# Optimization experiments

Measured on AMD Instinct MI355X. Metric: run time of the kernel, lower is better.

The kernel has to match this reference:

```python
import jax, jax.numpy as jnp
import numpy as np

N_HEAD = 16


def setup_inputs() -> dict:
    key = jax.random.key(0)
    ks = jax.random.split(key, 6)
    B, S, D = 2, 2048, 1024
    w = 0.02
    return {
        "x": jax.random.normal(ks[0], (B, S, D), dtype=jnp.float32),
        "attention_mask": jnp.ones((B, S), dtype=jnp.int32),
        "Wq": jax.random.normal(ks[1], (D, D), dtype=jnp.float32) * w,
        "bq": jnp.zeros((D,), dtype=jnp.float32),
        "Wk": jax.random.normal(ks[2], (D, D), dtype=jnp.float32) * w,
        "bk": jnp.zeros((D,), dtype=jnp.float32),
        "Wv": jax.random.normal(ks[3], (D, D), dtype=jnp.float32) * w,
        "bv": jnp.zeros((D,), dtype=jnp.float32),
        "Wp": jax.random.normal(ks[4], (D, D), dtype=jnp.float32) * w,
        "bp": jnp.zeros((D,), dtype=jnp.float32),
    }


def reference(x, attention_mask, Wq, bq, Wk, bk, Wv, bv, Wp, bp):
    # x: (B,S,D); PyTorch Linear: y = x @ W.T + b
    B, S, D = x.shape
    H = N_HEAD
    HD = D // H
    scale = 1.0 / jnp.sqrt(jnp.asarray(HD, dtype=x.dtype))

    def heads(W, b):
        return (x @ W.T + b).reshape(B, S, H, HD).transpose(0, 2, 1, 3)  # (B,H,S,HD)

    q = heads(Wq, bq)
    k = heads(Wk, bk)
    v = heads(Wv, bv)

    logits = jnp.einsum("bhsd,bhtd->bhst", q, k) * scale  # (B,H,S,S)

    causal = jnp.tril(jnp.ones((S, S), dtype=bool))  # (S,S)
    am = attention_mask.astype(bool)
    mask = causal[None, None, :, :] & (am[:, None, :, None] & am[:, None, None, :])

    float_min = jnp.finfo(x.dtype).min
    logits = jnp.where(mask, logits, float_min)
    w = jax.nn.softmax(logits, axis=-1)  # dropout is identity in eval / p=0

    attn = jnp.einsum("bhst,bhtd->bhsd", w, v)  # (B,H,S,HD)
    attn = attn.transpose(0, 2, 1, 3).reshape(B, S, D)
    return attn @ Wp.T + bp
```

## Files before the change

kernel.cpp:

```cpp
#include <hip/hip_runtime.h>


#define BB 2
#define SS 2048
#define DD 1024
#define HH 16
#define HDD 64
#define NEG_BIG (-1.0e30f)

typedef __attribute__((ext_vector_type(8))) short short8;
typedef __attribute__((ext_vector_type(4))) float floatx4;
typedef unsigned int u32;
#define AS_GLOBAL __attribute__((address_space(1)))
#define AS_LDS    __attribute__((address_space(3)))

__device__ __forceinline__ ushort f2bf(float f) {
    unsigned u = __float_as_uint(f);
    u += 0x7fffu + ((u >> 16) & 1u);
    return (ushort)(u >> 16);
}
__device__ __forceinline__ unsigned pk2(float a, float b) {
    return ((unsigned)f2bf(b) << 16) | (unsigned)f2bf(a);
}
__device__ __forceinline__ void storeT(float* p, float v) { *p = v; }
__device__ __forceinline__ void storeT(ushort* p, float v) { *p = f2bf(v); }

__device__ __forceinline__ void dma16(void* lds, const void* g) {
    __builtin_amdgcn_global_load_lds((const AS_GLOBAL u32*)g, (AS_LDS u32*)lds,
                                     16, 0, 0);
}

__global__ __launch_bounds__(256) void cvt_all(
    const float* __restrict__ x, const float* __restrict__ wq,
    const float* __restrict__ wk, const float* __restrict__ wv,
    ushort* __restrict__ dst)
{
    const size_t g = (size_t)blockIdx.x * 256 + threadIdx.x;
    const size_t flat = g * 8;
    const float* s;
    size_t off;
    if (flat < (size_t)4194304)      { s = x;  off = flat; }
    else if (flat < (size_t)5242880) { s = wq; off = flat - 4194304; }
    else if (flat < (size_t)6291456) { s = wk; off = flat - 5242880; }
    else                             { s = wv; off = flat - 6291456; }
    const float4 a = ((const float4*)(s + off))[0];
    const float4 b = ((const float4*)(s + off))[1];
    uint4 u;
    u.x = pk2(a.x, a.y); u.y = pk2(a.z, a.w);
    u.z = pk2(b.x, b.y); u.w = pk2(b.z, b.w);
    *(uint4*)(dst + flat) = u;
}

template <int QKV, typename TW, typename TO>
__global__ __launch_bounds__(256) void gemm_mfma(
    const ushort* __restrict__ A,
    const TW* __restrict__ W0, const TW* __restrict__ W1,
    const TW* __restrict__ W2,
    const float* __restrict__ B0, const float* __restrict__ B1,
    const float* __restrict__ B2,
    TO* __restrict__ O0, TO* __restrict__ O1, TO* __restrict__ O2)
{
    __shared__ ushort As[128 * 32];
    __shared__ ushort Bs[128 * 32];
    __shared__ float bias_s[128];

    const TW* W;
    const float* bias;
    TO* out;
    int z = 0;
    if (QKV) {
        z = blockIdx.z;
        W    = z == 0 ? W0 : (z == 1 ? W1 : W2);
        bias = z == 0 ? B0 : (z == 1 ? B1 : B2);
        out  = z == 0 ? O0 : (z == 1 ? O1 : O2);
    } else { W = W0; bias = B0; out = O0; }

    const int tid = threadIdx.x;
    const int bm = blockIdx.x * 128, bn = blockIdx.y * 128;
    const int wave = tid >> 6, lane = tid & 63, quad = lane >> 4, lm = lane & 15;
    const int wm = wave >> 1, wn = wave & 1;
    const int r0 = tid >> 2, c0 = (tid & 3) * 8;

    if (tid < 128) bias_s[tid] = bias[bn + tid];

    const floatx4 zz = {0.f, 0.f, 0.f, 0.f};
    floatx4 acc[4][4];
#pragma unroll
    for (int i = 0; i < 4; ++i)
#pragma unroll
        for (int j = 0; j < 4; ++j) acc[i][j] = zz;

    for (int k0 = 0; k0 < DD; k0 += 32) {
        __syncthreads();
        dma16(&As[r0 * 32 + c0], A + (size_t)(bm + r0) * DD + k0 + c0);
        dma16(&As[(64 + r0) * 32 + c0], A + (size_t)(bm + 64 + r0) * DD + k0 + c0);
        if constexpr (sizeof(TW) == 2) {
            dma16(&Bs[r0 * 32 + c0],
                  (const ushort*)W + (size_t)(bn + r0) * DD + k0 + c0);
            dma16(&Bs[(64 + r0) * 32 + c0],
                  (const ushort*)W + (size_t)(bn + 64 + r0) * DD + k0 + c0);
        } else {
#pragma unroll
            for (int hh = 0; hh < 2; ++hh) {
                const float* wr = (const float*)W
                    + (size_t)(bn + hh * 64 + r0) * DD + k0 + c0;
                const float4 a = ((const float4*)wr)[0];
                const float4 b = ((const float4*)wr)[1];
                uint4 u;
                u.x = pk2(a.x, a.y); u.y = pk2(a.z, a.w);
                u.z = pk2(b.x, b.y); u.w = pk2(b.z, b.w);
                *(uint4*)&Bs[(hh * 64 + r0) * 32 + c0] = u;
            }
        }
        __syncthreads();

        short8 af[4], bf[4];
#pragma unroll
        for (int i = 0; i < 4; ++i)
            af[i] = *(const short8*)&As[(wm * 64 + i * 16 + lm) * 32 + quad * 8];
#pragma unroll
        for (int j = 0; j < 4; ++j)
            bf[j] = *(const short8*)&Bs[(wn * 64 + j * 16 + lm) * 32 + quad * 8];
#pragma unroll
        for (int i = 0; i < 4; ++i)
#pragma unroll
            for (int j = 0; j < 4; ++j)
                acc[i][j] = __builtin_amdgcn_mfma_f32_16x16x32_bf16(
                    af[i], bf[j], acc[i][j], 0, 0, 0);
    }

#pragma unroll
    for (int i = 0; i < 4; ++i) {
#pragma unroll
        for (int j = 0; j < 4; ++j) {
            const int nl = wn * 64 + j * 16 + lm;
            const int n = bn + nl;
            const float bb = bias_s[nl];
#pragma unroll
            for (int r = 0; r < 4; ++r) {
                const int m = bm + wm * 64 + i * 16 + quad * 4 + r;
                const float v = acc[i][j][r] + bb;
                size_t oidx;
                if (QKV) {
                    const int b = m >> 11, s = m & 2047, h = n >> 6, hd = n & 63;
                    if (z == 2)
                        oidx = (((size_t)(b * HH + h) * HDD) + hd) * SS + s;
                    else
                        oidx = (((size_t)(b * HH + h) * SS) + s) * HDD + hd;
                } else {
                    oidx = (size_t)m * DD + n;
                }
                storeT(out + oidx, v);
            }
        }
    }
}

__global__ __launch_bounds__(256) void attn_mfma(
    const ushort* __restrict__ Q, const ushort* __restrict__ K,
    const ushort* __restrict__ Vt, const int* __restrict__ am,
    ushort* __restrict__ O)
{
    __shared__ ushort Ks[64 * 72];
    __shared__ ushort Vts[64 * 72];
    __shared__ ushort Ps[4][32 * 72];

    const int tid = threadIdx.x;
    const int wq = tid >> 6, lane = tid & 63, quad = lane >> 4, lm = lane & 15;
    const int qt = (int)(gridDim.x - 1 - blockIdx.x);
    const int bh = blockIdx.y, b = bh >> 4, h = bh & 15;
    const size_t base = (size_t)bh * SS * HDD;
    const size_t tbase = (size_t)bh * HDD * SS;
    const int* amrow = am + b * SS;
    const int q0 = qt * 128 + wq * 32;

    short8 qf[2][2];
#pragma unroll
    for (int sub = 0; sub < 2; ++sub) {
        const ushort* qp = Q + base + (size_t)(q0 + sub * 16 + lm) * HDD + quad * 8;
        qf[sub][0] = *(const short8*)qp;
        qf[sub][1] = *(const short8*)(qp + 32);
    }
    int amq[2][4];
#pragma unroll
    for (int sub = 0; sub < 2; ++sub)
#pragma unroll
        for (int r = 0; r < 4; ++r)
            amq[sub][r] = amrow[q0 + sub * 16 + quad * 4 + r];

    const floatx4 zz = {0.f, 0.f, 0.f, 0.f};
    floatx4 o_acc[2][4];
#pragma unroll
    for (int sub = 0; sub < 2; ++sub)
#pragma unroll
        for (int n2 = 0; n2 < 4; ++n2) o_acc[sub][n2] = zz;
    float l_r[2][4] = {};

    const int sr = tid >> 2, sc = (tid & 3) * 16;
    const int ktmax = 2 * qt + 1;

    for (int kt = 0; kt <= ktmax; ++kt) {
        __syncthreads();
        {
            const ushort* kp = K + base + (size_t)(kt * 64 + sr) * HDD + sc;
            const uint4 u0 = ((const uint4*)kp)[0], u1 = ((const uint4*)kp)[1];
            *(uint4*)&Ks[sr * 72 + sc] = u0;
            *(uint4*)&Ks[sr * 72 + sc + 8] = u1;
        }
        {
            const ushort* vp = Vt + tbase + (size_t)sr * SS + kt * 64 + sc;
            const uint4 u0 = ((const uint4*)vp)[0], u1 = ((const uint4*)vp)[1];
            *(uint4*)&Vts[sr * 72 + sc] = u0;
            *(uint4*)&Vts[sr * 72 + sc + 8] = u1;
        }
        __syncthreads();

        int amk4[4];
#pragma unroll
        for (int nt = 0; nt < 4; ++nt) amk4[nt] = amrow[kt * 64 + nt * 16 + lm];

#pragma unroll
        for (int nt = 0; nt < 4; ++nt) {
            const short8 kf0 = *(const short8*)&Ks[(nt * 16 + lm) * 72 + quad * 8];
            const short8 kf1 = *(const short8*)&Ks[(nt * 16 + lm) * 72 + 32 + quad * 8];
            const int tg = kt * 64 + nt * 16 + lm;
#pragma unroll
            for (int sub = 0; sub < 2; ++sub) {
                floatx4 s = zz;
                s = __builtin_amdgcn_mfma_f32_16x16x32_bf16(qf[sub][0], kf0, s, 0, 0, 0);
                s = __builtin_amdgcn_mfma_f32_16x16x32_bf16(qf[sub][1], kf1, s, 0, 0, 0);
#pragma unroll
                for (int r = 0; r < 4; ++r) {
                    const int qg = q0 + sub * 16 + quad * 4 + r;
                    float sv = s[r] * 0.125f;
                    const bool ok = amk4[nt] && amq[sub][r] && (tg <= qg);
                    sv = ok ? sv : NEG_BIG;
                    const float e = __expf(fminf(sv, 30.f));
                    l_r[sub][r] += e;
                    Ps[wq][(sub * 16 + quad * 4 + r) * 72 + nt * 16 + lm] = f2bf(e);
                }
            }
        }

        short8 af[2][2];
#pragma unroll
        for (int sub = 0; sub < 2; ++sub) {
            af[sub][0] = *(const short8*)&Ps[wq][(sub * 16 + lm) * 72 + quad * 8];
            af[sub][1] = *(const short8*)&Ps[wq][(sub * 16 + lm) * 72 + 32 + quad * 8];
        }
#pragma unroll
        for (int n2 = 0; n2 < 4; ++n2) {
            const short8 vf0 = *(const short8*)&Vts[(n2 * 16 + lm) * 72 + quad * 8];
            const short8 vf1 = *(const short8*)&Vts[(n2 * 16 + lm) * 72 + 32 + quad * 8];
#pragma unroll
            for (int sub = 0; sub < 2; ++sub) {
                o_acc[sub][n2] = __builtin_amdgcn_mfma_f32_16x16x32_bf16(
                    af[sub][0], vf0, o_acc[sub][n2], 0, 0, 0);
                o_acc[sub][n2] = __builtin_amdgcn_mfma_f32_16x16x32_bf16(
                    af[sub][1], vf1, o_acc[sub][n2], 0, 0, 0);
            }
        }
    }

#pragma unroll
    for (int sub = 0; sub < 2; ++sub) {
        float inv[4];
#pragma unroll
        for (int r = 0; r < 4; ++r) {
            float l = l_r[sub][r];
            l += __shfl_xor(l, 1);
            l += __shfl_xor(l, 2);
            l += __shfl_xor(l, 4);
            l += __shfl_xor(l, 8);
            inv[r] = l > 0.f ? 1.f / l : 0.f;
        }
#pragma unroll
        for (int n2 = 0; n2 < 4; ++n2)
#pragma unroll
            for (int r = 0; r < 4; ++r) {
                const int s = q0 + sub * 16 + quad * 4 + r;
                O[((size_t)(b * SS + s)) * DD + h * HDD + n2 * 16 + lm] =
                    f2bf(o_acc[sub][n2][r] * inv[r]);
            }
    }
}

extern "C" void kernel_launch(void* const* d_in, const int* in_sizes, int n_in,
                              void* d_out, int out_size, void* d_ws, size_t ws_size,
                              hipStream_t stream) {
    const float* x  = (const float*)d_in[0];
    const int*   am = (const int*)d_in[1];
    const float* Wq = (const float*)d_in[2];
    const float* bq = (const float*)d_in[3];
    const float* Wk = (const float*)d_in[4];
    const float* bk = (const float*)d_in[5];
    const float* Wv = (const float*)d_in[6];
    const float* bv = (const float*)d_in[7];
    const float* Wp = (const float*)d_in[8];
    const float* bp = (const float*)d_in[9];
    float* out = (float*)d_out;

    const size_t elems = (size_t)BB * HH * SS * HDD;
    ushort* q_ws = (ushort*)d_ws;
    ushort* k_ws = q_ws + elems;
    ushort* v_ws = k_ws + elems;
    ushort* a_ws = v_ws + elems;

    ushort* xb  = (ushort*)d_out;
    ushort* wqb = xb + 4194304;
    ushort* wkb = wqb + 1048576;
    ushort* wvb = wkb + 1048576;

    cvt_all<<<3584, 256, 0, stream>>>(x, Wq, Wk, Wv, xb);

    gemm_mfma<1, ushort, ushort><<<dim3(32, 8, 3), 256, 0, stream>>>(
        xb, wqb, wkb, wvb, bq, bk, bv, q_ws, k_ws, v_ws);

    attn_mfma<<<dim3(SS / 128, BB * HH), 256, 0, stream>>>(q_ws, k_ws, v_ws, am, a_ws);

    gemm_mfma<0, float, float><<<dim3(32, 8, 1), 256, 0, stream>>>(
        a_ws, Wp, Wp, Wp, bp, bp, bp, out, out, out);
}
```

Before: 251.9 us.

## Split attention over key tiles into two partitions and add a combine kernel

Attention now splits each query tile's key loop across two blocks (even and odd key tiles). Each block writes an unnormalized partial output and row sums, and a new combine kernel sums the two partials and normalizes. This doubles the grid to improve occupancy and load balance, at the cost of an extra pass over partial outputs. The MFMA operands are also swapped so each lane holds 4 contiguous columns, which enables vectorized ushort4/float4 stores in the GEMM epilogues and attention output. The V projection is split into its own GEMM launch with a vectorized transposed store, and the key mask is staged through LDS.

```diff
diff --git a/kernel.cpp b/kernel.cpp
--- a/kernel.cpp
+++ b/kernel.cpp
@@ -22,9 +22,16 @@
 __device__ __forceinline__ unsigned pk2(float a, float b) {
     return ((unsigned)f2bf(b) << 16) | (unsigned)f2bf(a);
 }
-__device__ __forceinline__ void storeT(float* p, float v) { *p = v; }
-__device__ __forceinline__ void storeT(ushort* p, float v) { *p = f2bf(v); }
-
+__device__ __forceinline__ void unpack8(const uint4 u, float* d) {
+    d[0] = __uint_as_float(u.x << 16);
+    d[1] = __uint_as_float(u.x & 0xffff0000u);
+    d[2] = __uint_as_float(u.y << 16);
+    d[3] = __uint_as_float(u.y & 0xffff0000u);
+    d[4] = __uint_as_float(u.z << 16);
+    d[5] = __uint_as_float(u.z & 0xffff0000u);
+    d[6] = __uint_as_float(u.w << 16);
+    d[7] = __uint_as_float(u.w & 0xffff0000u);
+}
 __device__ __forceinline__ void dma16(void* lds, const void* g) {
     __builtin_amdgcn_global_load_lds((const AS_GLOBAL u32*)g, (AS_LDS u32*)lds,
                                      16, 0, 0);
@@ -35,8 +42,7 @@
     const float* __restrict__ wk, const float* __restrict__ wv,
     ushort* __restrict__ dst)
 {
-    const size_t g = (size_t)blockIdx.x * 256 + threadIdx.x;
-    const size_t flat = g * 8;
+    const size_t flat = ((size_t)blockIdx.x * 256 + threadIdx.x) * 8;
     const float* s;
     size_t off;
     if (flat < (size_t)4194304)      { s = x;  off = flat; }
@@ -51,29 +57,21 @@
     *(uint4*)(dst + flat) = u;
 }
 
-template <int QKV, typename TW, typename TO>
+template <int MODE, typename TW, typename TO>
 __global__ __launch_bounds__(256) void gemm_mfma(
     const ushort* __restrict__ A,
     const TW* __restrict__ W0, const TW* __restrict__ W1,
-    const TW* __restrict__ W2,
     const float* __restrict__ B0, const float* __restrict__ B1,
-    const float* __restrict__ B2,
-    TO* __restrict__ O0, TO* __restrict__ O1, TO* __restrict__ O2)
+    TO* __restrict__ O0, TO* __restrict__ O1)
 {
     __shared__ ushort As[128 * 32];
     __shared__ ushort Bs[128 * 32];
     __shared__ float bias_s[128];
 
-    const TW* W;
-    const float* bias;
-    TO* out;
-    int z = 0;
-    if (QKV) {
-        z = blockIdx.z;
-        W    = z == 0 ? W0 : (z == 1 ? W1 : W2);
-        bias = z == 0 ? B0 : (z == 1 ? B1 : B2);
-        out  = z == 0 ? O0 : (z == 1 ? O1 : O2);
-    } else { W = W0; bias = B0; out = O0; }
+    const TW* W = W0;
+    const float* bias = B0;
+    TO* out = O0;
+    if (MODE == 1 && blockIdx.z == 1) { W = W1; bias = B1; out = O1; }
 
     const int tid = threadIdx.x;
     const int bm = blockIdx.x * 128, bn = blockIdx.y * 128;
@@ -124,33 +122,52 @@
 #pragma unroll
         for (int i = 0; i < 4; ++i)
 #pragma unroll
-            for (int j = 0; j < 4; ++j)
-                acc[i][j] = __builtin_amdgcn_mfma_f32_16x16x32_bf16(
-                    af[i], bf[j], acc[i][j], 0, 0, 0);
+            for (int j = 0; j < 4; ++j) {
+                if (MODE == 2)
+                    acc[i][j] = __builtin_amdgcn_mfma_f32_16x16x32_bf16(
+                        af[i], bf[j], acc[i][j], 0, 0, 0);
+                else
+                    acc[i][j] = __builtin_amdgcn_mfma_f32_16x16x32_bf16(
+                        bf[j], af[i], acc[i][j], 0, 0, 0);
+            }
     }
 
 #pragma unroll
     for (int i = 0; i < 4; ++i) {
 #pragma unroll
         for (int j = 0; j < 4; ++j) {
-            const int nl = wn * 64 + j * 16 + lm;
-            const int n = bn + nl;
-            const float bb = bias_s[nl];
-#pragma unroll
-            for (int r = 0; r < 4; ++r) {
-                const int m = bm + wm * 64 + i * 16 + quad * 4 + r;
-                const float v = acc[i][j][r] + bb;
-                size_t oidx;
-                if (QKV) {
+            if (MODE == 2) {
+                const int n = bn + wn * 64 + j * 16 + lm;
+                const int m0 = bm + wm * 64 + i * 16 + quad * 4;
+                const int b = m0 >> 11, s0 = m0 & 2047;
+                const float bb = bias_s[n - bn];
+                ushort4 v;
+                v.x = f2bf(acc[i][j][0] + bb);
+                v.y = f2bf(acc[i][j][1] + bb);
+                v.z = f2bf(acc[i][j][2] + bb);
+                v.w = f2bf(acc[i][j][3] + bb);
+                *(ushort4*)((ushort*)out + ((size_t)(b * DD + n)) * SS + s0) = v;
+            } else {
+                const int nl = wn * 64 + j * 16 + quad * 4;
+                const int n = bn + nl;
+                const int m = bm + wm * 64 + i * 16 + lm;
+                if (MODE == 1) {
                     const int b = m >> 11, s = m & 2047, h = n >> 6, hd = n & 63;
-                    if (z == 2)
-                        oidx = (((size_t)(b * HH + h) * HDD) + hd) * SS + s;
-                    else
-                        oidx = (((size_t)(b * HH + h) * SS) + s) * HDD + hd;
+                    ushort4 v;
+                    v.x = f2bf(acc[i][j][0] + bias_s[nl + 0]);
+                    v.y = f2bf(acc[i][j][1] + bias_s[nl + 1]);
+                    v.z = f2bf(acc[i][j][2] + bias_s[nl + 2]);
+                    v.w = f2bf(acc[i][j][3] + bias_s[nl + 3]);
+                    *(ushort4*)((ushort*)out
+                        + (((size_t)(b * HH + h) * SS) + s) * HDD + hd) = v;
                 } else {
-                    oidx = (size_t)m * DD + n;
+                    float4 v;
+                    v.x = acc[i][j][0] + bias_s[nl + 0];
+                    v.y = acc[i][j][1] + bias_s[nl + 1];
+                    v.z = acc[i][j][2] + bias_s[nl + 2];
+                    v.w = acc[i][j][3] + bias_s[nl + 3];
+                    *(float4*)((float*)out + (size_t)m * DD + n) = v;
                 }
-                storeT(out + oidx, v);
             }
         }
     }
@@ -159,16 +176,18 @@
 __global__ __launch_bounds__(256) void attn_mfma(
     const ushort* __restrict__ Q, const ushort* __restrict__ K,
     const ushort* __restrict__ Vt, const int* __restrict__ am,
-    ushort* __restrict__ O)
+    ushort* __restrict__ Opart, float* __restrict__ lbuf)
 {
     __shared__ ushort Ks[64 * 72];
     __shared__ ushort Vts[64 * 72];
     __shared__ ushort Ps[4][32 * 72];
+    __shared__ int amk_s[64];
 
     const int tid = threadIdx.x;
     const int wq = tid >> 6, lane = tid & 63, quad = lane >> 4, lm = lane & 15;
     const int qt = (int)(gridDim.x - 1 - blockIdx.x);
     const int bh = blockIdx.y, b = bh >> 4, h = bh & 15;
+    const int split = blockIdx.z;
     const size_t base = (size_t)bh * SS * HDD;
     const size_t tbase = (size_t)bh * HDD * SS;
     const int* amrow = am + b * SS;
@@ -181,12 +200,9 @@
         qf[sub][0] = *(const short8*)qp;
         qf[sub][1] = *(const short8*)(qp + 32);
     }
-    int amq[2][4];
-#pragma unroll
-    for (int sub = 0; sub < 2; ++sub)
-#pragma unroll
-        for (int r = 0; r < 4; ++r)
-            amq[sub][r] = amrow[q0 + sub * 16 + quad * 4 + r];
+    int amq[2];
+#pragma unroll
+    for (int sub = 0; sub < 2; ++sub) amq[sub] = amrow[q0 + sub * 16 + lm];
 
     const floatx4 zz = {0.f, 0.f, 0.f, 0.f};
     floatx4 o_acc[2][4];
@@ -194,12 +210,12 @@
     for (int sub = 0; sub < 2; ++sub)
 #pragma unroll
         for (int n2 = 0; n2 < 4; ++n2) o_acc[sub][n2] = zz;
-    float l_r[2][4] = {};
+    float l_lane[2] = {0.f, 0.f};
 
     const int sr = tid >> 2, sc = (tid & 3) * 16;
     const int ktmax = 2 * qt + 1;
 
-    for (int kt = 0; kt <= ktmax; ++kt) {
+    for (int kt = split; kt <= ktmax; kt += 2) {
         __syncthreads();
         {
             const ushort* kp = K + base + (size_t)(kt * 64 + sr) * HDD + sc;
@@ -213,32 +229,36 @@
             *(uint4*)&Vts[sr * 72 + sc] = u0;
             *(uint4*)&Vts[sr * 72 + sc + 8] = u1;
         }
+        if (tid < 64) amk_s[tid] = amrow[kt * 64 + tid];
         __syncthreads();
-
-        int amk4[4];
-#pragma unroll
-        for (int nt = 0; nt < 4; ++nt) amk4[nt] = amrow[kt * 64 + nt * 16 + lm];
 
 #pragma unroll
         for (int nt = 0; nt < 4; ++nt) {
             const short8 kf0 = *(const short8*)&Ks[(nt * 16 + lm) * 72 + quad * 8];
             const short8 kf1 = *(const short8*)&Ks[(nt * 16 + lm) * 72 + 32 + quad * 8];
-            const int tg = kt * 64 + nt * 16 + lm;
+            const int4 amk4 = *(const int4*)&amk_s[nt * 16 + quad * 4];
 #pragma unroll
             for (int sub = 0; sub < 2; ++sub) {
                 floatx4 s = zz;
-                s = __builtin_amdgcn_mfma_f32_16x16x32_bf16(qf[sub][0], kf0, s, 0, 0, 0);
-                s = __builtin_amdgcn_mfma_f32_16x16x32_bf16(qf[sub][1], kf1, s, 0, 0, 0);
-#pragma unroll
-                for (int r = 0; r < 4; ++r) {
-                    const int qg = q0 + sub * 16 + quad * 4 + r;
-                    float sv = s[r] * 0.125f;
-                    const bool ok = amk4[nt] && amq[sub][r] && (tg <= qg);
-                    sv = ok ? sv : NEG_BIG;
-                    const float e = __expf(fminf(sv, 30.f));
-                    l_r[sub][r] += e;
-                    Ps[wq][(sub * 16 + quad * 4 + r) * 72 + nt * 16 + lm] = f2bf(e);
+                s = __builtin_amdgcn_mfma_f32_16x16x32_bf16(kf0, qf[sub][0], s, 0, 0, 0);
+                s = __builtin_amdgcn_mfma_f32_16x16x32_bf16(kf1, qf[sub][1], s, 0, 0, 0);
+                const int qg = q0 + sub * 16 + lm;
+                const int t0 = kt * 64 + nt * 16 + quad * 4;
+                float e0, e1, e2, e3;
+                {
+                    const bool ok0 = amk4.x && amq[sub] && (t0 + 0 <= qg);
+                    const bool ok1 = amk4.y && amq[sub] && (t0 + 1 <= qg);
+                    const bool ok2 = amk4.z && amq[sub] && (t0 + 2 <= qg);
+                    const bool ok3 = amk4.w && amq[sub] && (t0 + 3 <= qg);
+                    e0 = __expf(fminf(ok0 ? s[0] * 0.125f : NEG_BIG, 30.f));
+                    e1 = __expf(fminf(ok1 ? s[1] * 0.125f : NEG_BIG, 30.f));
+                    e2 = __expf(fminf(ok2 ? s[2] * 0.125f : NEG_BIG, 30.f));
+                    e3 = __expf(fminf(ok3 ? s[3] * 0.125f : NEG_BIG, 30.f));
                 }
+                l_lane[sub] += (e0 + e1) + (e2 + e3);
+                ushort4 pv;
+                pv.x = f2bf(e0); pv.y = f2bf(e1); pv.z = f2bf(e2); pv.w = f2bf(e3);
+                *(ushort4*)&Ps[wq][(sub * 16 + lm) * 72 + nt * 16 + quad * 4] = pv;
             }
         }
 
@@ -255,34 +275,56 @@
 #pragma unroll
             for (int sub = 0; sub < 2; ++sub) {
                 o_acc[sub][n2] = __builtin_amdgcn_mfma_f32_16x16x32_bf16(
-                    af[sub][0], vf0, o_acc[sub][n2], 0, 0, 0);
+                    vf0, af[sub][0], o_acc[sub][n2], 0, 0, 0);
                 o_acc[sub][n2] = __builtin_amdgcn_mfma_f32_16x16x32_bf16(
-                    af[sub][1], vf1, o_acc[sub][n2], 0, 0, 0);
+                    vf1, af[sub][1], o_acc[sub][n2], 0, 0, 0);
             }
         }
     }
 
 #pragma unroll
     for (int sub = 0; sub < 2; ++sub) {
-        float inv[4];
-#pragma unroll
-        for (int r = 0; r < 4; ++r) {
-            float l = l_r[sub][r];
-            l += __shfl_xor(l, 1);
-            l += __shfl_xor(l, 2);
-            l += __shfl_xor(l, 4);
-            l += __shfl_xor(l, 8);
-            inv[r] = l > 0.f ? 1.f / l : 0.f;
-        }
-#pragma unroll
-        for (int n2 = 0; n2 < 4; ++n2)
-#pragma unroll
-            for (int r = 0; r < 4; ++r) {
-                const int s = q0 + sub * 16 + quad * 4 + r;
-                O[((size_t)(b * SS + s)) * DD + h * HDD + n2 * 16 + lm] =
-                    f2bf(o_acc[sub][n2][r] * inv[r]);
-            }
-    }
+        float l = l_lane[sub];
+        l += __shfl_xor(l, 16);
+        l += __shfl_xor(l, 32);
+        if (quad == 0)
+            lbuf[(size_t)split * (BB * HH * SS) + (size_t)bh * SS + q0 + sub * 16 + lm] = l;
+        const int srow = q0 + sub * 16 + lm;
+#pragma unroll
+        for (int n2 = 0; n2 < 4; ++n2) {
+            ushort4 v;
+            v.x = f2bf(o_acc[sub][n2][0]);
+            v.y = f2bf(o_acc[sub][n2][1]);
+            v.z = f2bf(o_acc[sub][n2][2]);
+            v.w = f2bf(o_acc[sub][n2][3]);
+            *(ushort4*)(Opart + (size_t)split * (BB * SS * DD)
+                        + ((size_t)(b * SS + srow)) * DD + h * HDD + n2 * 16 + quad * 4) = v;
+        }
+    }
+}
+
+__global__ __launch_bounds__(256) void combine(
+    const ushort* __restrict__ Opart, const float* __restrict__ lbuf,
+    ushort* __restrict__ Aout)
+{
+    const size_t e = ((size_t)blockIdx.x * 256 + threadIdx.x) * 8;
+    const int m = (int)(e >> 10);
+    const int col = (int)(e & 1023);
+    const int b = m >> 11, s = m & 2047, h = col >> 6;
+    const float l = lbuf[(b * HH + h) * SS + s]
+                  + lbuf[BB * HH * SS + (b * HH + h) * SS + s];
+    const float inv = l > 0.f ? 1.f / l : 0.f;
+    const uint4 u0 = *(const uint4*)(Opart + e);
+    const uint4 u1 = *(const uint4*)(Opart + (size_t)BB * SS * DD + e);
+    float f0[8], f1[8];
+    unpack8(u0, f0);
+    unpack8(u1, f1);
+    uint4 o;
+    o.x = pk2((f0[0] + f1[0]) * inv, (f0[1] + f1[1]) * inv);
+    o.y = pk2((f0[2] + f1[2]) * inv, (f0[3] + f1[3]) * inv);
+    o.z = pk2((f0[4] + f1[4]) * inv, (f0[5] + f1[5]) * inv);
+    o.w = pk2((f0[6] + f1[6]) * inv, (f0[7] + f1[7]) * inv);
+    *(uint4*)(Aout + e) = o;
 }
 
 extern "C" void kernel_launch(void* const* d_in, const int* in_sizes, int n_in,
@@ -304,7 +346,7 @@
     ushort* q_ws = (ushort*)d_ws;
     ushort* k_ws = q_ws + elems;
     ushort* v_ws = k_ws + elems;
-    ushort* a_ws = v_ws + elems;
+    float*  lbuf = (float*)(v_ws + elems);
 
     ushort* xb  = (ushort*)d_out;
     ushort* wqb = xb + 4194304;
@@ -313,11 +355,18 @@
 
     cvt_all<<<3584, 256, 0, stream>>>(x, Wq, Wk, Wv, xb);
 
-    gemm_mfma<1, ushort, ushort><<<dim3(32, 8, 3), 256, 0, stream>>>(
-        xb, wqb, wkb, wvb, bq, bk, bv, q_ws, k_ws, v_ws);
-
-    attn_mfma<<<dim3(SS / 128, BB * HH), 256, 0, stream>>>(q_ws, k_ws, v_ws, am, a_ws);
+    gemm_mfma<1, ushort, ushort><<<dim3(32, 8, 2), 256, 0, stream>>>(
+        xb, wqb, wkb, bq, bk, q_ws, k_ws);
+    gemm_mfma<2, ushort, ushort><<<dim3(32, 8, 1), 256, 0, stream>>>(
+        xb, wvb, (const ushort*)nullptr, bv, (const float*)nullptr,
+        v_ws, (ushort*)nullptr);
+
+    attn_mfma<<<dim3(SS / 128, BB * HH, 2), 256, 0, stream>>>(
+        q_ws, k_ws, v_ws, am, (ushort*)d_out, lbuf);
+
+    combine<<<2048, 256, 0, stream>>>((const ushort*)d_out, lbuf, q_ws);
 
     gemm_mfma<0, float, float><<<dim3(32, 8, 1), 256, 0, stream>>>(
-        a_ws, Wp, Wp, Wp, bp, bp, bp, out, out, out);
-}
+        q_ws, Wp, (const float*)nullptr, bp, (const float*)nullptr,
+        out, (float*)nullptr);
+}
```

New measurement: 251.3 us. About the same (-0.3%).
